# Kernel optimization log

Measured on AMD Instinct MI355X. Metric: run time of the kernel, lower is better.

## Reference

```python
import jax, jax.numpy as jnp
import numpy as np

N_NODES = 100000
N_EDGES = 1600000
D_IN = 64
D_OUT = 64


def setup_inputs() -> dict:
    key = jax.random.key(0)
    k1, k2, k3, k4, k5, k6, k7 = jax.random.split(key, 7)
    x = jax.random.normal(k1, (N_NODES, D_IN), dtype=jnp.float32)
    edge_index = jax.random.randint(k2, (2, N_EDGES), 0, N_NODES, dtype=jnp.int64)
    pos_encoding = jax.random.normal(k3, (N_NODES, D_IN), dtype=jnp.float32)
    # GCNConv linear weight (no bias inside lin; bias added post-aggregation)
    W_gcn = jax.random.normal(k4, (D_IN, D_OUT), dtype=jnp.float32) / np.sqrt(D_IN)
    b_gcn = jax.random.normal(k5, (D_OUT,), dtype=jnp.float32) * 0.01
    # positional encoding Linear
    W_pos = jax.random.normal(k6, (D_IN, D_OUT), dtype=jnp.float32) / np.sqrt(D_IN)
    b_pos = jax.random.normal(k7, (D_OUT,), dtype=jnp.float32) * 0.01
    return {"x": x, "edge_index": edge_index, "pos_encoding": pos_encoding,
            "W_gcn": W_gcn, "b_gcn": b_gcn, "W_pos": W_pos, "b_pos": b_pos}


def _gcn_conv(x, edge_index, W, b):
    n = x.shape[0]
    # add self-loops (PyG GCNConv default)
    loop = jnp.arange(n, dtype=edge_index.dtype)
    src = jnp.concatenate([edge_index[0], loop])
    dst = jnp.concatenate([edge_index[1], loop])
    # symmetric normalization: deg over destination with unit edge weights
    deg = jax.ops.segment_sum(jnp.ones_like(src, dtype=x.dtype), dst, num_segments=n)
    dinv = jnp.where(deg > 0, jax.lax.rsqrt(deg), 0.0)
    norm = dinv[src] * dinv[dst]  # [E+N]
    h = x @ W  # [N, D_OUT]
    msg = h[src] * norm[:, None]  # gather + scale
    out = jax.ops.segment_sum(msg, dst, num_segments=n)  # scatter-add
    return out + b


def reference(x, edge_index, pos_encoding, W_gcn, b_gcn, W_pos, b_pos):
    conv_out = _gcn_conv(x, edge_index, W_gcn, b_gcn)
    pos = pos_encoding @ W_pos + b_pos
    return conv_out + pos
```

## Files before the change

kernel.cpp:

```cpp
#include <hip/hip_runtime.h>
#include <hip/hip_fp16.h>

#define NN 100000
#define NE 1600000
#define D  64

#define B1   1024
#define BSH  8
#define BMSK 255
#define NB   391
#define CAP  4864

typedef __attribute__((ext_vector_type(8))) _Float16 f16x8;
typedef __attribute__((ext_vector_type(4))) float    f32x4;

__global__ __launch_bounds__(256) void k_hist(const int* __restrict__ dst,
                                              int* __restrict__ hist) {
    __shared__ int h[NB];
    int t = threadIdx.x, blk = blockIdx.x;
    for (int i = t; i < NB; i += 256) h[i] = 0;
    __syncthreads();
    for (int e = blk * 256 + t; e < NE; e += B1 * 256)
        atomicAdd(&h[dst[e] >> BSH], 1);
    __syncthreads();
    for (int i = t; i < NB; i += 256) hist[i * B1 + blk] = h[i];
}

__global__ __launch_bounds__(1024) void k_scanA(int* __restrict__ hist,
                                                int* __restrict__ bsum) {
    __shared__ int ps[1024];
    int t = threadIdx.x, b = blockIdx.x;
    int v = hist[b * B1 + t];
    ps[t] = v;
    __syncthreads();
    for (int off = 1; off < 1024; off <<= 1) {
        int u = (t >= off) ? ps[t - off] : 0;
        __syncthreads();
        ps[t] += u;
        __syncthreads();
    }
    hist[b * B1 + t] = ps[t] - v;
    if (t == 1023) bsum[b] = ps[t];
}

__global__ __launch_bounds__(512) void k_scanB(const int* __restrict__ bsum,
                                               int* __restrict__ binoff) {
    __shared__ int ps[512];
    int t = threadIdx.x;
    int v = (t < NB) ? bsum[t] : 0;
    ps[t] = v;
    __syncthreads();
    for (int off = 1; off < 512; off <<= 1) {
        int u = (t >= off) ? ps[t - off] : 0;
        __syncthreads();
        ps[t] += u;
        __syncthreads();
    }
    if (t < NB) binoff[t] = ps[t] - v;
    if (t == NB - 1) binoff[NB] = ps[t];
}

__global__ __launch_bounds__(256) void k_scatter1(
    const int* __restrict__ src, const int* __restrict__ dst,
    const int* __restrict__ hist, const int* __restrict__ binoff,
    unsigned* __restrict__ ebuf)
{
    __shared__ int cur[NB];
    int t = threadIdx.x, blk = blockIdx.x;
    for (int i = t; i < NB; i += 256)
        cur[i] = binoff[i] + hist[i * B1 + blk];
    __syncthreads();
    for (int e = blk * 256 + t; e < NE; e += B1 * 256) {
        int d = dst[e];
        int p = atomicAdd(&cur[d >> BSH], 1);
        ebuf[p] = ((unsigned)src[e] << BSH) | (unsigned)(d & BMSK);
    }
}

__global__ __launch_bounds__(512) void k_build(
    const int* __restrict__ binoff, const unsigned* __restrict__ ebuf,
    int* __restrict__ rs, float* __restrict__ dinv, int* __restrict__ bucket)
{
    __shared__ unsigned cache[CAP];
    __shared__ int c[256];
    __shared__ int ps[256];
    int t = threadIdx.x, b = blockIdx.x;
    int e0 = binoff[b], e1 = binoff[b + 1];
    int cnt = e1 - e0;
    if (t < 256) c[t] = 0;
    __syncthreads();
    for (int i = t; i < cnt; i += 512) {
        unsigned u = ebuf[e0 + i];
        if (i < CAP) cache[i] = u;
        atomicAdd(&c[u & BMSK], 1);
    }
    __syncthreads();
    int a = (t < 256) ? c[t] : 0;
    if (t < 256) ps[t] = a;
    __syncthreads();
    for (int off = 1; off < 256; off <<= 1) {
        int u2 = (t >= off && t < 256) ? ps[t - off] : 0;
        __syncthreads();
        if (t < 256) ps[t] += u2;
        __syncthreads();
    }
    if (t < 256) {
        int p = e0 + ps[t] - a;
        int node = (b << BSH) + t;
        if (node < NN) { rs[node] = p; dinv[node] = rsqrtf((float)(a + 1)); }
        c[t] = p;
    }
    if (b == NB - 1 && t == 0) rs[NN] = NE;
    __syncthreads();
    for (int i = t; i < cnt; i += 512) {
        unsigned u = (i < CAP) ? cache[i] : ebuf[e0 + i];
        int pp = atomicAdd(&c[u & BMSK], 1);
        bucket[pp] = (int)(u >> BSH);
    }
}

__global__ __launch_bounds__(256) void k_mm(
    const float* __restrict__ x, const float* __restrict__ Wg,
    const float* __restrict__ dinv, __half* __restrict__ g,
    const float* __restrict__ pos, const float* __restrict__ Wp,
    const float* __restrict__ bg, const float* __restrict__ bp,
    float* __restrict__ out)
{
    __shared__ __align__(16) _Float16 Wt[64][64];
    int t = threadIdx.x;
    int lane = t & 63;
    int wid = t >> 6;
    int half_grid = gridDim.x >> 1;
    bool job2 = blockIdx.x >= half_grid;
    int blk = job2 ? (blockIdx.x - half_grid) : blockIdx.x;
    const float* A = job2 ? pos : x;
    const float* W = job2 ? Wp : Wg;

    if (blockIdx.x == 0 && t < 64) g[(long)NN * D + t] = __float2half(0.f);

    for (int i = t; i < 64 * 64; i += 256) {
        int k = i >> 6, n = i & 63;
        Wt[n][k] = (_Float16)W[i];
    }
    __syncthreads();

    int lr = lane & 15;
    int lg = lane >> 4;
    int kofs = lg * 8;

    f16x8 b[4][2];
#pragma unroll
    for (int n = 0; n < 4; ++n)
#pragma unroll
        for (int kt = 0; kt < 2; ++kt)
            b[n][kt] = *(const f16x8*)&Wt[n * 16 + lr][kt * 32 + kofs];

    float bsum[4] = {0.f, 0.f, 0.f, 0.f};
    if (job2) {
#pragma unroll
        for (int n = 0; n < 4; ++n) {
            int cc = n * 16 + lr;
            bsum[n] = bg[cc] + bp[cc];
        }
    }

    for (int rb0 = blk * 64; rb0 < NN; rb0 += half_grid * 64) {
        int rb = rb0 + wid * 16;
        int arow = rb + lr;
        int arc = arow < NN ? arow : NN - 1;
        const float4* ap = (const float4*)(A + (long)arc * 64 + kofs);
        float4 p0 = ap[0], p1 = ap[1], p2 = ap[8], p3 = ap[9];
        f16x8 a0, a1;
        a0[0] = (_Float16)p0.x; a0[1] = (_Float16)p0.y;
        a0[2] = (_Float16)p0.z; a0[3] = (_Float16)p0.w;
        a0[4] = (_Float16)p1.x; a0[5] = (_Float16)p1.y;
        a0[6] = (_Float16)p1.z; a0[7] = (_Float16)p1.w;
        a1[0] = (_Float16)p2.x; a1[1] = (_Float16)p2.y;
        a1[2] = (_Float16)p2.z; a1[3] = (_Float16)p2.w;
        a1[4] = (_Float16)p3.x; a1[5] = (_Float16)p3.y;
        a1[6] = (_Float16)p3.z; a1[7] = (_Float16)p3.w;

        f32x4 z = {0.f, 0.f, 0.f, 0.f};
        f32x4 acc[4] = {z, z, z, z};
#pragma unroll
        for (int n = 0; n < 4; ++n) {
            acc[n] = __builtin_amdgcn_mfma_f32_16x16x32_f16(a0, b[n][0], acc[n], 0, 0, 0);
            acc[n] = __builtin_amdgcn_mfma_f32_16x16x32_f16(a1, b[n][1], acc[n], 0, 0, 0);
        }

        int orow0 = rb + lg * 4;
        if (!job2) {
#pragma unroll
            for (int r = 0; r < 4; ++r) {
                int row = orow0 + r;
                if (row < NN) {
                    float di = dinv[row];
#pragma unroll
                    for (int n = 0; n < 4; ++n)
                        g[(long)row * D + n * 16 + lr] = __float2half(acc[n][r] * di);
                }
            }
        } else {
#pragma unroll
            for (int r = 0; r < 4; ++r) {
                int row = orow0 + r;
                if (row < NN) {
#pragma unroll
                    for (int n = 0; n < 4; ++n)
                        out[(long)row * D + n * 16 + lr] = acc[n][r] + bsum[n];
                }
            }
        }
    }
}

__global__ __launch_bounds__(256) void k_gather(
    const int* __restrict__ rs, const int* __restrict__ bucket,
    const float* __restrict__ dinv, const __half* __restrict__ g,
    float* __restrict__ out)
{
    int lane = threadIdx.x & 63;
    int f = lane & 7;
    int grp = lane >> 3;
    int w0 = (blockIdx.x << 2) + (threadIdx.x >> 6);
    int nw = gridDim.x << 2;
    const uint4* gq = (const uint4*)g;

    for (int n0 = w0; n0 < NN; n0 += nw) {
        int node = __builtin_amdgcn_readfirstlane(n0);
        int r0 = rs[node], r1 = rs[node + 1];
        float a0 = 0.f, a1 = 0.f, a2 = 0.f, a3 = 0.f;
        float a4 = 0.f, a5 = 0.f, a6 = 0.f, a7 = 0.f;
        for (int base = r0; base < r1; base += 64) {
            int rem = r1 - base;
            int nl = rem < 64 ? rem : 64;
            int sl = (lane < nl) ? bucket[base + lane] : NN;
            int NG = (nl + 7) >> 3;
#pragma unroll 4
            for (int c = 0; c < NG; ++c) {
                int s = __shfl(sl, c * 8 + grp);
                uint4 u = gq[(long)s * 8 + f];
                __half2 h0 = *(__half2*)&u.x, h1 = *(__half2*)&u.y;
                __half2 h2 = *(__half2*)&u.z, h3 = *(__half2*)&u.w;
                a0 += __low2float(h0); a1 += __high2float(h0);
                a2 += __low2float(h1); a3 += __high2float(h1);
                a4 += __low2float(h2); a5 += __high2float(h2);
                a6 += __low2float(h3); a7 += __high2float(h3);
            }
        }
#pragma unroll
        for (int mask = 8; mask <= 32; mask <<= 1) {
            a0 += __shfl_xor(a0, mask); a1 += __shfl_xor(a1, mask);
            a2 += __shfl_xor(a2, mask); a3 += __shfl_xor(a3, mask);
            a4 += __shfl_xor(a4, mask); a5 += __shfl_xor(a5, mask);
            a6 += __shfl_xor(a6, mask); a7 += __shfl_xor(a7, mask);
        }
        if (lane < 16) {
            int ff = lane & 7, hs = lane >> 3;
            uint4 u = gq[(long)node * 8 + ff];
            __half2 s0 = hs ? *(__half2*)&u.z : *(__half2*)&u.x;
            __half2 s1 = hs ? *(__half2*)&u.w : *(__half2*)&u.y;
            float b0 = hs ? a4 : a0, b1 = hs ? a5 : a1;
            float b2 = hs ? a6 : a2, b3 = hs ? a7 : a3;
            float di = dinv[node];
            float4* op = (float4*)(out + (long)node * D) + (ff * 2 + hs);
            float4 o = *op;
            o.x += (b0 + __low2float(s0)) * di;
            o.y += (b1 + __high2float(s0)) * di;
            o.z += (b2 + __low2float(s1)) * di;
            o.w += (b3 + __high2float(s1)) * di;
            *op = o;
        }
    }
}

extern "C" void kernel_launch(void* const* d_in, const int* in_sizes, int n_in,
                              void* d_out, int out_size, void* d_ws, size_t ws_size,
                              hipStream_t stream) {
    const float* x   = (const float*)d_in[0];
    const int*   ei  = (const int*)d_in[1];
    const float* pos = (const float*)d_in[2];
    const float* Wg  = (const float*)d_in[3];
    const float* bg  = (const float*)d_in[4];
    const float* Wp  = (const float*)d_in[5];
    const float* bp  = (const float*)d_in[6];
    float* out = (float*)d_out;

    const int* src = ei;
    const int* dst = ei + NE;

    char* Wb = (char*)d_ws;
    unsigned* ebuf   = (unsigned*)Wb;
    __half*   g      = (__half*)(Wb + 6400000);
    int*      bucket = (int*)(Wb + 19200128);
    int*      hist   = bucket;
    int*      rs     = (int*)(Wb + 25600128);
    float*    dinv   = (float*)(rs + NN + 4);
    int*      bsum   = (int*)(dinv + NN);
    int*      binoff = bsum + 512;

    hipLaunchKernelGGL(k_hist,     dim3(B1),   dim3(256),  0, stream, dst, hist);
    hipLaunchKernelGGL(k_scanA,    dim3(NB),   dim3(1024), 0, stream, hist, bsum);
    hipLaunchKernelGGL(k_scanB,    dim3(1),    dim3(512),  0, stream, bsum, binoff);
    hipLaunchKernelGGL(k_scatter1, dim3(B1),   dim3(256),  0, stream,
                       src, dst, hist, binoff, ebuf);
    hipLaunchKernelGGL(k_build,    dim3(NB),   dim3(512),  0, stream,
                       binoff, ebuf, rs, dinv, bucket);
    hipLaunchKernelGGL(k_mm,       dim3(1564), dim3(256),  0, stream,
                       x, Wg, dinv, g, pos, Wp, bg, bp, out);
    hipLaunchKernelGGL(k_gather,   dim3(2048), dim3(256),  0, stream,
                       rs, bucket, dinv, g, out);
}
```

Before: 218.3 us.

## Fuse per-bin CSR sort into gather kernel and merge bin scans

The second-level bucket sort (per-node ordering within each 256-node bin) is moved out of a separate build kernel into the gather kernel. That kernel now sorts edges into shared memory and aggregates its bin's nodes directly, and a lightweight count kernel computes dinv beforehand. The hist layout is transposed so one scan kernel handles 8 bins per block, and the bin-offset scan is recomputed inside each consumer by one wave, which removes the scanB launch and the bucket/rs global arrays. The cost is far less gather parallelism (391 blocks of 1024 threads, each processing nodes with no cross-block balancing), an extra pass over ebuf for counting, and overflow beyond the shared cache written back into ebuf.

```diff
diff --git a/kernel.cpp b/kernel.cpp
--- a/kernel.cpp
+++ b/kernel.cpp
@@ -9,10 +9,37 @@
 #define BSH  8
 #define BMSK 255
 #define NB   391
-#define CAP  4864
+#define PAD  400
+#define CAPS 4864
 
 typedef __attribute__((ext_vector_type(8))) _Float16 f16x8;
 typedef __attribute__((ext_vector_type(4))) float    f32x4;
+
+__device__ __forceinline__ void scan_bsum_wave0(const int* __restrict__ bsum,
+                                                int* binoff_l, int t) {
+    if (t < 64) {
+        int base = t * 7;
+        int loc[7]; int run = 0;
+#pragma unroll
+        for (int j = 0; j < 7; ++j) {
+            int idx = base + j;
+            int v = (idx < NB) ? bsum[idx] : 0;
+            loc[j] = run; run += v;
+        }
+        int pre = run;
+#pragma unroll
+        for (int off = 1; off < 64; off <<= 1) {
+            int u = __shfl_up(pre, off);
+            if (t >= off) pre += u;
+        }
+        pre -= run;
+#pragma unroll
+        for (int j = 0; j < 7; ++j) {
+            int idx = base + j;
+            if (idx <= NB) binoff_l[idx] = pre + loc[j];
+        }
+    }
+}
 
 __global__ __launch_bounds__(256) void k_hist(const int* __restrict__ dst,
                                               int* __restrict__ hist) {
@@ -23,52 +50,51 @@
     for (int e = blk * 256 + t; e < NE; e += B1 * 256)
         atomicAdd(&h[dst[e] >> BSH], 1);
     __syncthreads();
-    for (int i = t; i < NB; i += 256) hist[i * B1 + blk] = h[i];
-}
-
-__global__ __launch_bounds__(1024) void k_scanA(int* __restrict__ hist,
+    for (int i = t; i < NB; i += 256) hist[blk * PAD + i] = h[i];
+}
+
+__global__ __launch_bounds__(1024) void k_scanT(int* __restrict__ hist,
                                                 int* __restrict__ bsum) {
-    __shared__ int ps[1024];
-    int t = threadIdx.x, b = blockIdx.x;
-    int v = hist[b * B1 + t];
-    ps[t] = v;
+    __shared__ int ps[8][1024];
+    int t = threadIdx.x, b0 = blockIdx.x * 8;
+    int v[8];
+#pragma unroll
+    for (int j = 0; j < 8; ++j) {
+        v[j] = (b0 + j < NB) ? hist[t * PAD + b0 + j] : 0;
+        ps[j][t] = v[j];
+    }
     __syncthreads();
     for (int off = 1; off < 1024; off <<= 1) {
-        int u = (t >= off) ? ps[t - off] : 0;
+        int u[8];
+#pragma unroll
+        for (int j = 0; j < 8; ++j) u[j] = (t >= off) ? ps[j][t - off] : 0;
         __syncthreads();
-        ps[t] += u;
+#pragma unroll
+        for (int j = 0; j < 8; ++j) ps[j][t] += u[j];
         __syncthreads();
     }
-    hist[b * B1 + t] = ps[t] - v;
-    if (t == 1023) bsum[b] = ps[t];
-}
-
-__global__ __launch_bounds__(512) void k_scanB(const int* __restrict__ bsum,
-                                               int* __restrict__ binoff) {
-    __shared__ int ps[512];
-    int t = threadIdx.x;
-    int v = (t < NB) ? bsum[t] : 0;
-    ps[t] = v;
-    __syncthreads();
-    for (int off = 1; off < 512; off <<= 1) {
-        int u = (t >= off) ? ps[t - off] : 0;
-        __syncthreads();
-        ps[t] += u;
-        __syncthreads();
-    }
-    if (t < NB) binoff[t] = ps[t] - v;
-    if (t == NB - 1) binoff[NB] = ps[t];
+#pragma unroll
+    for (int j = 0; j < 8; ++j)
+        if (b0 + j < NB) hist[t * PAD + b0 + j] = ps[j][t] - v[j];
+    if (t == 1023) {
+#pragma unroll
+        for (int j = 0; j < 8; ++j)
+            if (b0 + j < NB) bsum[b0 + j] = ps[j][t];
+    }
 }
 
 __global__ __launch_bounds__(256) void k_scatter1(
     const int* __restrict__ src, const int* __restrict__ dst,
-    const int* __restrict__ hist, const int* __restrict__ binoff,
+    const int* __restrict__ hist, const int* __restrict__ bsum,
     unsigned* __restrict__ ebuf)
 {
     __shared__ int cur[NB];
+    __shared__ int binoff_l[NB + 1];
     int t = threadIdx.x, blk = blockIdx.x;
+    scan_bsum_wave0(bsum, binoff_l, t);
+    __syncthreads();
     for (int i = t; i < NB; i += 256)
-        cur[i] = binoff[i] + hist[i * B1 + blk];
+        cur[i] = binoff_l[i] + hist[blk * PAD + i];
     __syncthreads();
     for (int e = blk * 256 + t; e < NE; e += B1 * 256) {
         int d = dst[e];
@@ -77,45 +103,22 @@
     }
 }
 
-__global__ __launch_bounds__(512) void k_build(
-    const int* __restrict__ binoff, const unsigned* __restrict__ ebuf,
-    int* __restrict__ rs, float* __restrict__ dinv, int* __restrict__ bucket)
-{
-    __shared__ unsigned cache[CAP];
+__global__ __launch_bounds__(512) void k_count(const int* __restrict__ bsum,
+                                               const unsigned* __restrict__ ebuf,
+                                               float* __restrict__ dinv) {
     __shared__ int c[256];
-    __shared__ int ps[256];
+    __shared__ int binoff_l[NB + 1];
     int t = threadIdx.x, b = blockIdx.x;
-    int e0 = binoff[b], e1 = binoff[b + 1];
-    int cnt = e1 - e0;
+    scan_bsum_wave0(bsum, binoff_l, t);
     if (t < 256) c[t] = 0;
     __syncthreads();
-    for (int i = t; i < cnt; i += 512) {
-        unsigned u = ebuf[e0 + i];
-        if (i < CAP) cache[i] = u;
-        atomicAdd(&c[u & BMSK], 1);
-    }
-    __syncthreads();
-    int a = (t < 256) ? c[t] : 0;
-    if (t < 256) ps[t] = a;
-    __syncthreads();
-    for (int off = 1; off < 256; off <<= 1) {
-        int u2 = (t >= off && t < 256) ? ps[t - off] : 0;
-        __syncthreads();
-        if (t < 256) ps[t] += u2;
-        __syncthreads();
-    }
+    int e0 = binoff_l[b], e1 = binoff_l[b + 1];
+    for (int e = e0 + t; e < e1; e += 512)
+        atomicAdd(&c[ebuf[e] & BMSK], 1);
+    __syncthreads();
     if (t < 256) {
-        int p = e0 + ps[t] - a;
         int node = (b << BSH) + t;
-        if (node < NN) { rs[node] = p; dinv[node] = rsqrtf((float)(a + 1)); }
-        c[t] = p;
-    }
-    if (b == NB - 1 && t == 0) rs[NN] = NE;
-    __syncthreads();
-    for (int i = t; i < cnt; i += 512) {
-        unsigned u = (i < CAP) ? cache[i] : ebuf[e0 + i];
-        int pp = atomicAdd(&c[u & BMSK], 1);
-        bucket[pp] = (int)(u >> BSH);
+        if (node < NN) dinv[node] = rsqrtf((float)(c[t] + 1));
     }
 }
 
@@ -155,12 +158,12 @@
         for (int kt = 0; kt < 2; ++kt)
             b[n][kt] = *(const f16x8*)&Wt[n * 16 + lr][kt * 32 + kofs];
 
-    float bsum[4] = {0.f, 0.f, 0.f, 0.f};
+    float bsv[4] = {0.f, 0.f, 0.f, 0.f};
     if (job2) {
 #pragma unroll
         for (int n = 0; n < 4; ++n) {
             int cc = n * 16 + lr;
-            bsum[n] = bg[cc] + bp[cc];
+            bsv[n] = bg[cc] + bp[cc];
         }
     }
 
@@ -207,46 +210,98 @@
                 if (row < NN) {
 #pragma unroll
                     for (int n = 0; n < 4; ++n)
-                        out[(long)row * D + n * 16 + lr] = acc[n][r] + bsum[n];
+                        out[(long)row * D + n * 16 + lr] = acc[n][r] + bsv[n];
                 }
             }
         }
     }
 }
 
-__global__ __launch_bounds__(256) void k_gather(
-    const int* __restrict__ rs, const int* __restrict__ bucket,
-    const float* __restrict__ dinv, const __half* __restrict__ g,
-    float* __restrict__ out)
+__global__ __launch_bounds__(1024) void k_gather(
+    const int* __restrict__ bsum, unsigned* __restrict__ ebuf,
+    const __half* __restrict__ g, float* __restrict__ out)
 {
-    int lane = threadIdx.x & 63;
+    __shared__ unsigned cache[CAPS];
+    __shared__ int c[256];
+    __shared__ int cur[256];
+    __shared__ int rs_l[257];
+    __shared__ int binoff_l[NB + 1];
+    int t = threadIdx.x, b = blockIdx.x;
+    int lane = t & 63, w = t >> 6;
+
+    scan_bsum_wave0(bsum, binoff_l, t);
+    if (t < 256) c[t] = 0;
+    __syncthreads();
+    int e0 = binoff_l[b];
+    int cnt = binoff_l[b + 1] - e0;
+
+    for (int i = t; i < cnt; i += 1024) {
+        unsigned u = ebuf[e0 + i];
+        if (i < CAPS) cache[i] = u;
+        atomicAdd(&c[u & BMSK], 1);
+    }
+    __syncthreads();
+
+    if (t < 64) {
+        int base = t * 4;
+        int loc[4]; int run = 0;
+#pragma unroll
+        for (int j = 0; j < 4; ++j) { loc[j] = run; run += c[base + j]; }
+        int pre = run;
+#pragma unroll
+        for (int off = 1; off < 64; off <<= 1) {
+            int u = __shfl_up(pre, off);
+            if (t >= off) pre += u;
+        }
+        pre -= run;
+#pragma unroll
+        for (int j = 0; j < 4; ++j) {
+            rs_l[base + j] = pre + loc[j];
+            cur[base + j]  = pre + loc[j];
+        }
+        if (t == 63) rs_l[256] = pre + run;
+    }
+
+    unsigned ur[8]; int nmy = 0;
+    for (int i = t, j = 0; i < cnt && j < 8; i += 1024, ++j) {
+        ur[j] = (i < CAPS) ? cache[i] : ebuf[e0 + i];
+        nmy = j + 1;
+    }
+    __syncthreads();
+    for (int j = 0; j < nmy; ++j) {
+        unsigned u = ur[j];
+        int p = atomicAdd(&cur[u & BMSK], 1);
+        unsigned s = u >> BSH;
+        if (p < CAPS) cache[p] = s; else ebuf[e0 + p] = s;
+    }
+    __syncthreads();
+
     int f = lane & 7;
     int grp = lane >> 3;
-    int w0 = (blockIdx.x << 2) + (threadIdx.x >> 6);
-    int nw = gridDim.x << 2;
     const uint4* gq = (const uint4*)g;
-
-    for (int n0 = w0; n0 < NN; n0 += nw) {
-        int node = __builtin_amdgcn_readfirstlane(n0);
-        int r0 = rs[node], r1 = rs[node + 1];
+    for (int p = 0; p < 16; ++p) {
+        int r = p * 16 + w;
+        int node = (b << BSH) + r;
+        if (node >= NN) continue;
+        int rs0 = rs_l[r];
+        int nl = rs_l[r + 1] - rs0;
         float a0 = 0.f, a1 = 0.f, a2 = 0.f, a3 = 0.f;
         float a4 = 0.f, a5 = 0.f, a6 = 0.f, a7 = 0.f;
-        for (int base = r0; base < r1; base += 64) {
-            int rem = r1 - base;
-            int nl = rem < 64 ? rem : 64;
-            int sl = (lane < nl) ? bucket[base + lane] : NN;
-            int NG = (nl + 7) >> 3;
-#pragma unroll 4
-            for (int c = 0; c < NG; ++c) {
-                int s = __shfl(sl, c * 8 + grp);
-                uint4 u = gq[(long)s * 8 + f];
-                __half2 h0 = *(__half2*)&u.x, h1 = *(__half2*)&u.y;
-                __half2 h2 = *(__half2*)&u.z, h3 = *(__half2*)&u.w;
-                a0 += __low2float(h0); a1 += __high2float(h0);
-                a2 += __low2float(h1); a3 += __high2float(h1);
-                a4 += __low2float(h2); a5 += __high2float(h2);
-                a6 += __low2float(h3); a7 += __high2float(h3);
+        int NG = (nl + 7) >> 3;
+        for (int c2 = 0; c2 < NG; ++c2) {
+            int idx = c2 * 8 + grp;
+            int s = NN;
+            if (idx < nl) {
+                int ii = rs0 + idx;
+                s = (ii < CAPS) ? (int)cache[ii] : (int)ebuf[e0 + ii];
             }
+            uint4 u = gq[(long)s * 8 + f];
+            __half2 h0 = *(__half2*)&u.x, h1 = *(__half2*)&u.y;
+            __half2 h2 = *(__half2*)&u.z, h3 = *(__half2*)&u.w;
+            a0 += __low2float(h0); a1 += __high2float(h0);
+            a2 += __low2float(h1); a3 += __high2float(h1);
+            a4 += __low2float(h2); a5 += __high2float(h2);
+            a6 += __low2float(h3); a7 += __high2float(h3);
         }
 #pragma unroll
         for (int mask = 8; mask <= 32; mask <<= 1) {
@@ -262,7 +317,7 @@
             __half2 s1 = hs ? *(__half2*)&u.w : *(__half2*)&u.y;
             float b0 = hs ? a4 : a0, b1 = hs ? a5 : a1;
             float b2 = hs ? a6 : a2, b3 = hs ? a7 : a3;
-            float di = dinv[node];
+            float di = rsqrtf((float)(c[r] + 1));
             float4* op = (float4*)(out + (long)node * D) + (ff * 2 + hs);
             float4 o = *op;
             o.x += (b0 + __low2float(s0)) * di;
@@ -290,24 +345,20 @@
     const int* dst = ei + NE;
 
     char* Wb = (char*)d_ws;
-    unsigned* ebuf   = (unsigned*)Wb;
-    __half*   g      = (__half*)(Wb + 6400000);
-    int*      bucket = (int*)(Wb + 19200128);
-    int*      hist   = bucket;
-    int*      rs     = (int*)(Wb + 25600128);
-    float*    dinv   = (float*)(rs + NN + 4);
-    int*      bsum   = (int*)(dinv + NN);
-    int*      binoff = bsum + 512;
+    unsigned* ebuf = (unsigned*)Wb;
+    __half*   g    = (__half*)(Wb + 6400000);
+    int*      hist = (int*)(Wb + 19200128);
+    int*      bsum = hist + B1 * PAD;
+    float*    dinv = (float*)(bsum + 512);
 
     hipLaunchKernelGGL(k_hist,     dim3(B1),   dim3(256),  0, stream, dst, hist);
-    hipLaunchKernelGGL(k_scanA,    dim3(NB),   dim3(1024), 0, stream, hist, bsum);
-    hipLaunchKernelGGL(k_scanB,    dim3(1),    dim3(512),  0, stream, bsum, binoff);
+    hipLaunchKernelGGL(k_scanT,    dim3(49),   dim3(1024), 0, stream, hist, bsum);
     hipLaunchKernelGGL(k_scatter1, dim3(B1),   dim3(256),  0, stream,
-                       src, dst, hist, binoff, ebuf);
-    hipLaunchKernelGGL(k_build,    dim3(NB),   dim3(512),  0, stream,
-                       binoff, ebuf, rs, dinv, bucket);
+                       src, dst, hist, bsum, ebuf);
+    hipLaunchKernelGGL(k_count,    dim3(NB),   dim3(512),  0, stream,
+                       bsum, ebuf, dinv);
     hipLaunchKernelGGL(k_mm,       dim3(1564), dim3(256),  0, stream,
                        x, Wg, dinv, g, pos, Wp, bg, bp, out);
-    hipLaunchKernelGGL(k_gather,   dim3(2048), dim3(256),  0, stream,
-                       rs, bucket, dinv, g, out);
-}
+    hipLaunchKernelGGL(k_gather,   dim3(NB),   dim3(1024), 0, stream,
+                       bsum, ebuf, g, out);
+}
```

After: 221.2 us. Within noise of the previous version (+1.3%).
